# Optimization experiments

Hardware: AMD Instinct MI355X
Metric: run time of the kernel (lower is better)

## Reference

```python
import jax, jax.numpy as jnp
import numpy as np

B, T, F, D, H, L, DFF, G = 4, 2048, 512, 1024, 16, 2, 4096, 16
WSCALE = 0.03  # ~1/sqrt(D) so activations stay well-conditioned


def setup_inputs() -> dict:
    key = jax.random.key(0)
    ks = iter(jax.random.split(key, 24))

    def w(shape):
        return jax.random.normal(next(ks), shape, jnp.float32) * WSCALE

    return {
        "x": jax.random.normal(next(ks), (B, T, F), jnp.float32),
        "proj_w": w((D, F)), "proj_b": jnp.zeros((D,), jnp.float32),
        "wq": w((L, D, D)), "wk": w((L, D, D)), "wv": w((L, D, D)),
        "bq": jnp.zeros((L, D), jnp.float32), "bk": jnp.zeros((L, D), jnp.float32), "bv": jnp.zeros((L, D), jnp.float32),
        "wo": w((L, D, D)), "bo": jnp.zeros((L, D), jnp.float32),
        "ln1_g": jnp.ones((L, D), jnp.float32), "ln1_b": jnp.zeros((L, D), jnp.float32),
        "ln2_g": jnp.ones((L, D), jnp.float32), "ln2_b": jnp.zeros((L, D), jnp.float32),
        "w1": w((L, DFF, D)), "b1": jnp.zeros((L, DFF), jnp.float32),
        "w2": w((L, D, DFF)), "b2": jnp.zeros((L, D), jnp.float32),
        "hw1": w((G, D, D)), "hb1": jnp.zeros((G, D), jnp.float32),
        "hw2": w((G, 2, D)), "hb2": jnp.zeros((G, 2), jnp.float32),
        "nhead": H,
    }


def _ln(x, g, b, eps=1e-5):
    m = x.mean(-1, keepdims=True)
    v = ((x - m) ** 2).mean(-1, keepdims=True)
    return (x - m) * jax.lax.rsqrt(v + eps) * g + b


def _pe(t, d):
    # sinusoidal positional encoding, shape (t, d) (d even -> sin/cos interleave)
    pos = jnp.arange(t, dtype=jnp.float32)[:, None]
    div = jnp.exp(jnp.arange(0, d, 2, dtype=jnp.float32) * (-np.log(10000.0) / d))
    ph = pos * div
    return jnp.stack([jnp.sin(ph), jnp.cos(ph)], axis=-1).reshape(t, d)


def reference(x, proj_w, proj_b, wq, wk, wv, bq, bk, bv, wo, bo,
              ln1_g, ln1_b, ln2_g, ln2_b, w1, b1, w2, b2,
              hw1, hb1, hw2, hb2, nhead):
    Bx, Tx, _ = x.shape
    Dm = proj_w.shape[0]
    dh = Dm // nhead
    h = x @ proj_w.T + proj_b + _pe(Tx, Dm)  # (B,T,D)
    for l in range(wq.shape[0]):  # post-norm encoder layers
        q = (h @ wq[l].T + bq[l]).reshape(Bx, Tx, nhead, dh)
        k = (h @ wk[l].T + bk[l]).reshape(Bx, Tx, nhead, dh)
        v = (h @ wv[l].T + bv[l]).reshape(Bx, Tx, nhead, dh)
        # explicit (non-fused) attention path, as forced by need_weights=True
        scores = jnp.einsum('bthd,bshd->bhts', q, k) / jnp.sqrt(jnp.float32(dh))
        attn = jax.nn.softmax(scores, axis=-1)  # (B,H,T,T)
        ctx = jnp.einsum('bhts,bshd->bthd', attn, v).reshape(Bx, Tx, Dm)
        h = _ln(h + ctx @ wo[l].T + bo[l], ln1_g[l], ln1_b[l])
        ff = jax.nn.relu(h @ w1[l].T + b1[l]) @ w2[l].T + b2[l]
        h = _ln(h + ff, ln2_g[l], ln2_b[l])
    hl = h[:, -1, :]  # last-token pooling, (B,D)
    z = jax.nn.relu(jnp.einsum('bd,gkd->bgk', hl, hw1) + hb1)  # per-sector hidden
    logits = jnp.einsum('bgk,gok->bgo', z, hw2) + hb2           # (B,G,2)
    return jax.nn.softmax(logits, axis=-1)
```

## Files before the change

### kernel.cpp

```cpp
#include <hip/hip_runtime.h>
#include <hip/hip_bf16.h>
#include <cstdint>
#include <cstddef>


typedef __bf16 bf16_t;
typedef __attribute__((ext_vector_type(8))) __bf16 bf16x8;
typedef __attribute__((ext_vector_type(4))) __bf16 bf16x4;
typedef __attribute__((ext_vector_type(4))) float f32x4;
typedef __attribute__((ext_vector_type(16))) float f32x16;
typedef __attribute__((ext_vector_type(2))) unsigned u32x2;
typedef __attribute__((ext_vector_type(4))) unsigned u32x4;

#define DEV __device__ __forceinline__
#define AS1 __attribute__((address_space(1)))
#define AS3 __attribute__((address_space(3)))

DEV void gload_lds16(const void* g, void* l) {
  __builtin_amdgcn_global_load_lds((AS1 void*)(g), (AS3 void*)(l), 16, 0, 0);
}

DEV const char* swz_ptr(const void* base, int row, int colb) {
  return (const char*)base + row * 128 + ((((colb >> 4) ^ (row & 7))) << 4) +
         (colb & 15);
}

DEV unsigned cvtpk(float lo, float hi) {
  unsigned r;
  asm("v_cvt_pk_bf16_f32 %0, %1, %2" : "=v"(r) : "v"(lo), "v"(hi));
  return r;
}
DEV void swap32(unsigned& a, unsigned& b) {
  u32x2 r = __builtin_amdgcn_permlane32_swap(a, b, false, false);
  a = r[0];
  b = r[1];
}
DEV bf16x8 mkfrag(unsigned w0, unsigned w1, unsigned w2, unsigned w3) {
  u32x4 v = {w0, w1, w2, w3};
  return __builtin_bit_cast(bf16x8, v);
}

__global__ __launch_bounds__(256) void f2b_kernel(const float* __restrict__ s,
                                                  bf16_t* __restrict__ d, int n4) {
  const int i = blockIdx.x * 256 + threadIdx.x;
  if (i >= n4) return;
  const float4 v = *(const float4*)&s[(size_t)i * 4];
  bf16x4 o = {(bf16_t)v.x, (bf16_t)v.y, (bf16_t)v.z, (bf16_t)v.w};
  *(bf16x4*)&d[(size_t)i * 4] = o;
}

__global__ __launch_bounds__(256) void bcat_kernel(const float* __restrict__ bq,
                                                   const float* __restrict__ bk,
                                                   const float* __restrict__ bv,
                                                   float* __restrict__ out) {
  const int idx = blockIdx.x * 256 + threadIdx.x;
  const int l = idx / 3072, r = idx - l * 3072;
  const int p = r >> 10, i = r & 1023;
  const float* s = (p == 0) ? bq : ((p == 1) ? bk : bv);
  out[idx] = s[l * 1024 + i];
}

__global__ __launch_bounds__(256) void pe_kernel(float* __restrict__ pe) {
  const int idx = blockIdx.x * 256 + threadIdx.x;
  const int t = idx >> 9, i = idx & 511;
  const float dv = __expf((float)(2 * i) * -0.008994473019508785f);
  const float ph = (float)t * dv;
  pe[(size_t)t * 1024 + 2 * i] = sinf(ph);
  pe[(size_t)t * 1024 + 2 * i + 1] = cosf(ph);
}

template <int EPI, int BM, int BN>
__global__ __launch_bounds__(BM == 256 ? 512 : 256, 2) void gemm9(
    const bf16_t* __restrict__ A, const bf16_t* __restrict__ W,
    const float* __restrict__ bias, bf16_t* __restrict__ outb,
    float* __restrict__ outf, const float* __restrict__ res32,
    const float* __restrict__ pe, int M, int N, int K) {
  constexpr int T = (BM == 256) ? 512 : 256;
  constexpr int RPC = T / 8;
  constexpr int NA = (BM * 128) / (T * 16);
  constexpr int NB = (BN * 128) / (T * 16);
  constexpr int LPT = NA + NB;
  constexpr bool WIDE = (BM == 256 && BN == 256);
  constexpr int MF = WIDE ? 8 : 4;
  constexpr int ASZ = BM * 128;
  constexpr int BUFSZ = (BM + BN) * 128;
  __shared__ char smem[2][BUFSZ];
  const int tid = threadIdx.x, wv = tid >> 6, ln = tid & 63;
  const int nwg = gridDim.x * gridDim.y;
  int bid = blockIdx.y * gridDim.x + blockIdx.x;
  bid = (bid & 7) * (nwg >> 3) + (bid >> 3);
  const int m0 = (bid / gridDim.x) * BM, n0 = (bid % gridDim.x) * BN;
  const int wrow = WIDE ? (wv >> 2) * 128 : (wv >> 1) * 64;
  const int wcol = WIDE ? (wv & 3) * 64 : (wv & 1) * 64;
  f32x4 acc[MF][4] = {};

  const int tp = tid ^ ((tid >> 3) & 7);
  const int srow = tp >> 3, sc8 = (tp & 7) * 8;
  const bf16_t* pa[NA];
  const bf16_t* pb[NB];
#pragma unroll
  for (int u = 0; u < NA; ++u) pa[u] = A + (size_t)(m0 + u * RPC + srow) * K + sc8;
#pragma unroll
  for (int u = 0; u < NB; ++u) pb[u] = W + (size_t)(n0 + u * RPC + srow) * K + sc8;
  const int wvb = wv * 1024;

  auto stage = [&](int s) {
    char* bA = &smem[s][0] + wvb;
    char* bB = &smem[s][ASZ] + wvb;
#pragma unroll
    for (int u = 0; u < NA; ++u) {
      gload_lds16(pa[u], bA + u * (T * 16));
      pa[u] += 64;
    }
#pragma unroll
    for (int u = 0; u < NB; ++u) {
      gload_lds16(pb[u], bB + u * (T * 16));
      pb[u] += 64;
    }
  };

  auto wait_lpt = [&]() {
    if constexpr (LPT == 8)
      asm volatile("s_waitcnt vmcnt(8)" ::: "memory");
    else
      asm volatile("s_waitcnt vmcnt(6)" ::: "memory");
  };

  const int NK = K >> 6;
  stage(0);
  stage(1);
  wait_lpt();
  __builtin_amdgcn_s_barrier();

  for (int kt = 0; kt < NK; ++kt) {
    const char* bA = &smem[kt & 1][0];
    const char* bB = &smem[kt & 1][ASZ];
#pragma unroll
    for (int ks = 0; ks < 2; ++ks) {
      const int cb = ks * 64 + (ln >> 4) * 16;
      bf16x8 bF[4];
#pragma unroll
      for (int n = 0; n < 4; ++n) {
        const int lb = (wcol + n * 16 + (ln & 15)) * 128 + cb;
        bF[n] = *(const bf16x8*)(bB + (lb ^ (((lb >> 7) & 7) << 4)));
      }
#pragma unroll
      for (int mh = 0; mh < 2; ++mh) {
        bf16x8 aF[MF / 2];
#pragma unroll
        for (int m = 0; m < MF / 2; ++m) {
          const int lb = (wrow + (mh * (MF / 2) + m) * 16 + (ln & 15)) * 128 + cb;
          aF[m] = *(const bf16x8*)(bA + (lb ^ (((lb >> 7) & 7) << 4)));
        }
        __builtin_amdgcn_s_setprio(1);
#pragma unroll
        for (int m = 0; m < MF / 2; ++m)
#pragma unroll
          for (int n = 0; n < 4; ++n)
            acc[mh * (MF / 2) + m][n] = __builtin_amdgcn_mfma_f32_16x16x32_bf16(
                aF[m], bF[n], acc[mh * (MF / 2) + m][n], 0, 0, 0);
        __builtin_amdgcn_s_setprio(0);
      }
    }
    __builtin_amdgcn_s_barrier();
    if (kt + 2 < NK) {
      stage(kt & 1);
      wait_lpt();
    } else if (kt + 1 < NK) {
      asm volatile("s_waitcnt vmcnt(0)" ::: "memory");
    }
    __builtin_amdgcn_s_barrier();
    __builtin_amdgcn_sched_barrier(0);
  }

  const int rr = (ln >> 4) * 4, cc = ln & 15;
#pragma unroll
  for (int m = 0; m < MF; ++m) {
    const int rowb = m0 + wrow + m * 16 + rr;
#pragma unroll
    for (int n = 0; n < 4; ++n) {
      const int col = n0 + wcol + n * 16 + cc;
      const float bv = bias[col];
#pragma unroll
      for (int r = 0; r < 4; ++r) {
        const int row = rowb + r;
        float v = acc[m][n][r] + bv;
        const size_t o = (size_t)row * N + col;
        if constexpr (EPI == 1) {
          v = fmaxf(v, 0.f);
          outb[o] = (bf16_t)v;
        } else if constexpr (EPI == 2) {
          v += pe[(size_t)(row & 2047) * 1024 + col];
          outb[o] = (bf16_t)v;
          outf[o] = v;
        } else if constexpr (EPI == 3) {
          v += res32[o];
          outf[o] = v;
        } else {
          outb[o] = (bf16_t)v;
        }
      }
    }
  }
}

__global__ __launch_bounds__(256) void ln_kernel(const float* __restrict__ pre,
                                                 const float* __restrict__ g,
                                                 const float* __restrict__ b,
                                                 bf16_t* __restrict__ h16,
                                                 float* __restrict__ h32) {
  const int row = blockIdx.x, tid = threadIdx.x;
  const size_t base = (size_t)row * 1024 + tid * 4;
  const float4 v = *(const float4*)&pre[base];
  float s = v.x + v.y + v.z + v.w;
  float s2 = v.x * v.x + v.y * v.y + v.z * v.z + v.w * v.w;
#pragma unroll
  for (int m = 1; m < 64; m <<= 1) {
    s += __shfl_xor(s, m);
    s2 += __shfl_xor(s2, m);
  }
  __shared__ float ls[4], ls2[4];
  if ((tid & 63) == 0) {
    ls[tid >> 6] = s;
    ls2[tid >> 6] = s2;
  }
  __syncthreads();
  s = ls[0] + ls[1] + ls[2] + ls[3];
  s2 = ls2[0] + ls2[1] + ls2[2] + ls2[3];
  const float mean = s * (1.f / 1024.f);
  const float var = s2 * (1.f / 1024.f) - mean * mean;
  const float rs = rsqrtf(var + 1e-5f);
  const float4 gv = *(const float4*)&g[tid * 4];
  const float4 bv = *(const float4*)&b[tid * 4];
  const float o0 = (v.x - mean) * rs * gv.x + bv.x;
  const float o1 = (v.y - mean) * rs * gv.y + bv.y;
  const float o2 = (v.z - mean) * rs * gv.z + bv.z;
  const float o3 = (v.w - mean) * rs * gv.w + bv.w;
  bf16x4 ob = {(bf16_t)o0, (bf16_t)o1, (bf16_t)o2, (bf16_t)o3};
  *(bf16x4*)&h16[base] = ob;
  float4 of = {o0, o1, o2, o3};
  *(float4*)&h32[base] = of;
}

__global__ __launch_bounds__(256) void transpose_v(const bf16_t* __restrict__ v,
                                                   bf16_t* __restrict__ vt) {
  __shared__ bf16_t tile[64][80];
  const int bh = blockIdx.y, t0 = blockIdx.x * 64;
  const int tid = threadIdx.x;
  const int b = bh >> 4;
  const size_t vbase = ((size_t)(b * 2048 + t0)) * 3072 + (bh & 15) * 64;
#pragma unroll
  for (int p = 0; p < 2; ++p) {
    const int chunk = p * 256 + tid;
    const int tr = chunk >> 3, c8 = (chunk & 7) * 8;
    *(bf16x8*)&tile[tr][c8] = *(const bf16x8*)&v[vbase + (size_t)tr * 3072 + c8];
  }
  __syncthreads();
  const int d = tid >> 2, t8 = (tid & 3) * 16;
  bf16_t tmp[16];
#pragma unroll
  for (int j = 0; j < 16; ++j) tmp[j] = tile[t8 + j][d];
  const size_t obase = ((size_t)bh * 64 + d) * 2048 + t0 + t8;
  *(bf16x8*)&vt[obase] = *(bf16x8*)&tmp[0];
  *(bf16x8*)&vt[obase + 8] = *(bf16x8*)&tmp[8];
}

__global__ __launch_bounds__(256, 4) void attn_kernel(const bf16_t* __restrict__ qkv,
                                                      const bf16_t* __restrict__ vt,
                                                      bf16_t* __restrict__ ctx) {
  constexpr float SCL = 0.18033688011112042f;
  constexpr int QS = 3072;
  __shared__ bf16_t lK[2][64 * 64];
  __shared__ bf16_t lV[2][64 * 64];
  const int tid = threadIdx.x, wv = tid >> 6, ln = tid & 63;
  const int nwg = gridDim.x * gridDim.y;
  int bid = blockIdx.y * gridDim.x + blockIdx.x;
  bid = (bid & 7) * (nwg >> 3) + (bid >> 3);
  const int bh = bid / gridDim.x, b = bh >> 4, h = bh & 15;
  const int q0 = (bid % gridDim.x) * 128 + wv * 32;
  const int lq = ln & 31, hi = ln >> 5;
  const bf16_t* qp = qkv + (size_t)(b * 2048 + q0 + lq) * QS + h * 64 + hi * 8;
  bf16x8 qF[4];
#pragma unroll
  for (int kk = 0; kk < 4; ++kk) qF[kk] = *(const bf16x8*)(qp + kk * 16);
  f32x16 O0 = {}, O1 = {};
  float m_q = -1e30f, l_q = 0.f;
  const int sr = tid >> 3;
  const int scS = ((tid & 7) ^ ((tid >> 3) & 7)) * 8;
  const bf16_t* kp0 = qkv + 1024 + (size_t)(b * 2048 + sr) * QS + h * 64 + scS;
  const bf16_t* kp1 = kp0 + (size_t)32 * QS;
  const bf16_t* vp0 = vt + (size_t)bh * 64 * 2048 + (size_t)sr * 2048 + scS;
  const bf16_t* vp1 = vp0 + 32 * 2048;

  auto stage = [&](int bufi) {
    char* dk = (char*)&lK[bufi][0] + wv * 1024;
    char* dv = (char*)&lV[bufi][0] + wv * 1024;
    gload_lds16(kp0, dk);
    gload_lds16(kp1, dk + 4096);
    gload_lds16(vp0, dv);
    gload_lds16(vp1, dv + 4096);
    kp0 += (size_t)64 * QS;
    kp1 += (size_t)64 * QS;
    vp0 += 64;
    vp1 += 64;
  };

  stage(0);
  asm volatile("s_waitcnt vmcnt(0)" ::: "memory");
  __builtin_amdgcn_s_barrier();

  for (int st = 0; st < 32; ++st) {
    const int cur = st & 1;
    if (st + 1 < 32) stage(cur ^ 1);
#pragma unroll
    for (int sb = 0; sb < 2; ++sb) {
      f32x16 s = {};
      __builtin_amdgcn_s_setprio(1);
#pragma unroll
      for (int kk = 0; kk < 4; ++kk) {
        const bf16x8 kf =
            *(const bf16x8*)swz_ptr(&lK[cur][0], sb * 32 + lq, kk * 32 + hi * 16);
        s = __builtin_amdgcn_mfma_f32_32x32x16_bf16(kf, qF[kk], s, 0, 0, 0);
      }
      __builtin_amdgcn_s_setprio(0);
      float t0 = fmaxf(fmaxf(s[0], s[1]), fmaxf(s[2], s[3]));
      float t1 = fmaxf(fmaxf(s[4], s[5]), fmaxf(s[6], s[7]));
      float t2 = fmaxf(fmaxf(s[8], s[9]), fmaxf(s[10], s[11]));
      float t3 = fmaxf(fmaxf(s[12], s[13]), fmaxf(s[14], s[15]));
      float mx = fmaxf(fmaxf(t0, t1), fmaxf(t2, t3)) * SCL;
      mx = fmaxf(mx, __shfl_xor(mx, 32));
      if (__any(mx > m_q + 8.f)) {
        const float mnew = fmaxf(m_q, mx);
        const float alpha = exp2f(m_q - mnew);
        m_q = mnew;
        l_q *= alpha;
#pragma unroll
        for (int r = 0; r < 16; ++r) {
          const float ar = __shfl(alpha, (r & 3) + 8 * (r >> 2) + 4 * hi);
          O0[r] *= ar;
          O1[r] *= ar;
        }
      }
      float ra = 0.f, rb = 0.f;
#pragma unroll
      for (int i = 0; i < 8; ++i) {
        s[i] = exp2f(fmaf(s[i], SCL, -m_q));
        ra += s[i];
        s[i + 8] = exp2f(fmaf(s[i + 8], SCL, -m_q));
        rb += s[i + 8];
      }
      float rsum = ra + rb;
      rsum += __shfl_xor(rsum, 32);
      l_q += rsum;
      unsigned A = cvtpk(s[0], s[1]), Bq = cvtpk(s[2], s[3]);
      unsigned C = cvtpk(s[4], s[5]), Dq = cvtpk(s[6], s[7]);
      unsigned A2 = cvtpk(s[8], s[9]), B2 = cvtpk(s[10], s[11]);
      unsigned C2 = cvtpk(s[12], s[13]), D2 = cvtpk(s[14], s[15]);
      swap32(A, C);
      swap32(Bq, Dq);
      swap32(A2, C2);
      swap32(B2, D2);
      const bf16x8 f0 = mkfrag(A, Bq, C, Dq);
      const bf16x8 f1 = mkfrag(A2, B2, C2, D2);
      __builtin_amdgcn_s_setprio(1);
      const bf16x8 va = *(const bf16x8*)swz_ptr(&lV[cur][0], lq, sb * 64 + hi * 16);
      const bf16x8 vb =
          *(const bf16x8*)swz_ptr(&lV[cur][0], lq, sb * 64 + 32 + hi * 16);
      const bf16x8 vc =
          *(const bf16x8*)swz_ptr(&lV[cur][0], 32 + lq, sb * 64 + hi * 16);
      const bf16x8 vd =
          *(const bf16x8*)swz_ptr(&lV[cur][0], 32 + lq, sb * 64 + 32 + hi * 16);
      O0 = __builtin_amdgcn_mfma_f32_32x32x16_bf16(f0, va, O0, 0, 0, 0);
      O0 = __builtin_amdgcn_mfma_f32_32x32x16_bf16(f1, vb, O0, 0, 0, 0);
      O1 = __builtin_amdgcn_mfma_f32_32x32x16_bf16(f0, vc, O1, 0, 0, 0);
      O1 = __builtin_amdgcn_mfma_f32_32x32x16_bf16(f1, vd, O1, 0, 0, 0);
      __builtin_amdgcn_s_setprio(0);
    }
    asm volatile("s_waitcnt vmcnt(0)" ::: "memory");
    __builtin_amdgcn_s_barrier();
    __builtin_amdgcn_sched_barrier(0);
  }
  const float invl = 1.f / l_q;
  const size_t obase = ((size_t)(b * 2048 + q0)) * 1024 + h * 64 + lq;
#pragma unroll
  for (int r = 0; r < 16; ++r) {
    const int qr = (r & 3) + 8 * (r >> 2) + 4 * hi;
    const float iv = __shfl(invl, qr);
    ctx[obase + (size_t)qr * 1024] = (bf16_t)(O0[r] * iv);
    ctx[obase + (size_t)qr * 1024 + 32] = (bf16_t)(O1[r] * iv);
  }
}

__global__ __launch_bounds__(256) void head_z(const float* __restrict__ h32,
                                              const float* __restrict__ hw1,
                                              const float* __restrict__ hb1,
                                              float* __restrict__ z) {
  const int g = blockIdx.x, slab = blockIdx.y;
  const int wv = threadIdx.x >> 6, ln = threadIdx.x & 63;
  float4 hl[4][4];
#pragma unroll
  for (int b = 0; b < 4; ++b)
#pragma unroll
    for (int c = 0; c < 4; ++c)
      hl[b][c] = *(const float4*)&h32[((size_t)b * 2048 + 2047) * 1024 + c * 256 + ln * 4];
  const int k0 = slab * 64 + wv * 16;
  for (int kk = 0; kk < 16; ++kk) {
    const int kq = k0 + kk;
    const float* wrow = hw1 + ((size_t)g * 1024 + kq) * 1024;
    float p[4] = {0, 0, 0, 0};
#pragma unroll
    for (int c = 0; c < 4; ++c) {
      const float4 w4 = *(const float4*)&wrow[c * 256 + ln * 4];
#pragma unroll
      for (int b = 0; b < 4; ++b)
        p[b] += w4.x * hl[b][c].x + w4.y * hl[b][c].y + w4.z * hl[b][c].z +
                w4.w * hl[b][c].w;
    }
#pragma unroll
    for (int m = 1; m < 64; m <<= 1)
#pragma unroll
      for (int b = 0; b < 4; ++b) p[b] += __shfl_xor(p[b], m);
    if (ln == 0) {
#pragma unroll
      for (int b = 0; b < 4; ++b)
        z[((size_t)b * 16 + g) * 1024 + kq] = fmaxf(p[b] + hb1[g * 1024 + kq], 0.f);
    }
  }
}

__global__ __launch_bounds__(64) void head_logits(const float* __restrict__ z,
                                                  const float* __restrict__ hw2,
                                                  const float* __restrict__ hb2,
                                                  float* __restrict__ out) {
  const int b = blockIdx.x, g = blockIdx.y, ln = threadIdx.x;
  const float* zr = z + ((size_t)b * 16 + g) * 1024;
  const float* w0 = hw2 + (size_t)g * 2048;
  const float* w1 = w0 + 1024;
  float p0 = 0.f, p1 = 0.f;
#pragma unroll
  for (int c = 0; c < 4; ++c) {
    const float4 zv = *(const float4*)&zr[c * 256 + ln * 4];
    const float4 a0 = *(const float4*)&w0[c * 256 + ln * 4];
    const float4 a1 = *(const float4*)&w1[c * 256 + ln * 4];
    p0 += zv.x * a0.x + zv.y * a0.y + zv.z * a0.z + zv.w * a0.w;
    p1 += zv.x * a1.x + zv.y * a1.y + zv.z * a1.z + zv.w * a1.w;
  }
#pragma unroll
  for (int m = 1; m < 64; m <<= 1) {
    p0 += __shfl_xor(p0, m);
    p1 += __shfl_xor(p1, m);
  }
  if (ln == 0) {
    const float l0 = p0 + hb2[g * 2], l1 = p1 + hb2[g * 2 + 1];
    const float mx = fmaxf(l0, l1);
    const float e0 = expf(l0 - mx), e1 = expf(l1 - mx);
    const float inv = 1.f / (e0 + e1);
    out[(size_t)b * 32 + g * 2] = e0 * inv;
    out[(size_t)b * 32 + g * 2 + 1] = e1 * inv;
  }
}

extern "C" void kernel_launch(void* const* d_in, const int* in_sizes, int n_in,
                              void* d_out, int out_size, void* d_ws, size_t ws_size,
                              hipStream_t stream) {
  const float* x = (const float*)d_in[0];
  const float* proj_w = (const float*)d_in[1];
  const float* proj_b = (const float*)d_in[2];
  const float* wq = (const float*)d_in[3];
  const float* wk = (const float*)d_in[4];
  const float* wvv = (const float*)d_in[5];
  const float* bq = (const float*)d_in[6];
  const float* bk = (const float*)d_in[7];
  const float* bv = (const float*)d_in[8];
  const float* wo = (const float*)d_in[9];
  const float* bo = (const float*)d_in[10];
  const float* ln1_g = (const float*)d_in[11];
  const float* ln1_b = (const float*)d_in[12];
  const float* ln2_g = (const float*)d_in[13];
  const float* ln2_b = (const float*)d_in[14];
  const float* w1 = (const float*)d_in[15];
  const float* b1 = (const float*)d_in[16];
  const float* w2 = (const float*)d_in[17];
  const float* b2 = (const float*)d_in[18];
  const float* hw1 = (const float*)d_in[19];
  const float* hb1 = (const float*)d_in[20];
  const float* hw2 = (const float*)d_in[21];
  const float* hb2 = (const float*)d_in[22];
  float* out = (float*)d_out;
  char* ws = (char*)d_ws;

  size_t o = 0;
  auto take = [&](size_t bytes) { size_t r = o; o += bytes; return r; };
  const size_t o_wqkv = take(12582912);
  const size_t o_wo = take(4194304);
  const size_t o_w1 = take(16777216);
  const size_t o_w2 = take(16777216);
  const size_t o_pw = take(1048576);
  const size_t o_h16 = take(16777216);
  const size_t o_h32 = take(33554432);
  const size_t o_pre = take(33554432);
  const size_t o_r4 = take(67108864);
  const size_t o_r5 = take(16777216);
  const size_t o_z = take(262144);
  const size_t o_bqkv = take(24576);

  bf16_t* wqkv16 = (bf16_t*)(ws + o_wqkv);
  bf16_t* wo16 = (bf16_t*)(ws + o_wo);
  bf16_t* w1_16 = (bf16_t*)(ws + o_w1);
  bf16_t* w2_16 = (bf16_t*)(ws + o_w2);
  bf16_t* pw16 = (bf16_t*)(ws + o_pw);
  bf16_t* h16 = (bf16_t*)(ws + o_h16);
  float* h32 = (float*)(ws + o_h32);
  float* pre32 = (float*)(ws + o_pre);
  bf16_t* qkv16 = (bf16_t*)(ws + o_r4);
  bf16_t* vT16 = (bf16_t*)(ws + o_r4 + 50331648);
  bf16_t* ff1 = (bf16_t*)(ws + o_r4);
  bf16_t* x16 = (bf16_t*)(ws + o_r5);
  float* pe32 = (float*)(ws + o_r5 + 8388608);
  bf16_t* ctx16 = (bf16_t*)(ws + o_r5);
  float* zbuf = (float*)(ws + o_z);
  float* bqkv = (float*)(ws + o_bqkv);

  f2b_kernel<<<4096, 256, 0, stream>>>(x, x16, 1048576);
  f2b_kernel<<<512, 256, 0, stream>>>(proj_w, pw16, 131072);
  for (int l = 0; l < 2; ++l) {
    f2b_kernel<<<1024, 256, 0, stream>>>(wq + (size_t)l * 1048576,
                                         wqkv16 + (size_t)(l * 3 + 0) * 1048576, 262144);
    f2b_kernel<<<1024, 256, 0, stream>>>(wk + (size_t)l * 1048576,
                                         wqkv16 + (size_t)(l * 3 + 1) * 1048576, 262144);
    f2b_kernel<<<1024, 256, 0, stream>>>(wvv + (size_t)l * 1048576,
                                         wqkv16 + (size_t)(l * 3 + 2) * 1048576, 262144);
  }
  f2b_kernel<<<2048, 256, 0, stream>>>(wo, wo16, 524288);
  f2b_kernel<<<8192, 256, 0, stream>>>(w1, w1_16, 2097152);
  f2b_kernel<<<8192, 256, 0, stream>>>(w2, w2_16, 2097152);
  bcat_kernel<<<24, 256, 0, stream>>>(bq, bk, bv, bqkv);
  pe_kernel<<<4096, 256, 0, stream>>>(pe32);

  gemm9<2, 128, 128><<<dim3(8, 64), 256, 0, stream>>>(x16, pw16, proj_b, h16, h32,
                                                      nullptr, pe32, 8192, 1024, 512);

  for (int l = 0; l < 2; ++l) {
    const bf16_t* wqkv_l = wqkv16 + (size_t)l * 3145728;
    const bf16_t* wo_l = wo16 + (size_t)l * 1048576;
    const bf16_t* w1_l = w1_16 + (size_t)l * 4194304;
    const bf16_t* w2_l = w2_16 + (size_t)l * 4194304;

    gemm9<0, 256, 128><<<dim3(24, 32), 512, 0, stream>>>(h16, wqkv_l, bqkv + l * 3072,
                                                         qkv16, nullptr, nullptr,
                                                         nullptr, 8192, 3072, 1024);
    transpose_v<<<dim3(32, 64), 256, 0, stream>>>(qkv16 + 2048, vT16);
    attn_kernel<<<dim3(16, 64), 256, 0, stream>>>(qkv16, vT16, ctx16);
    gemm9<3, 128, 128><<<dim3(8, 64), 256, 0, stream>>>(ctx16, wo_l, bo + l * 1024,
                                                        nullptr, pre32, h32, nullptr,
                                                        8192, 1024, 1024);
    ln_kernel<<<8192, 256, 0, stream>>>(pre32, ln1_g + l * 1024, ln1_b + l * 1024, h16,
                                        h32);
    gemm9<1, 256, 256><<<dim3(16, 32), 512, 0, stream>>>(h16, w1_l, b1 + l * 4096, ff1,
                                                         nullptr, nullptr, nullptr,
                                                         8192, 4096, 1024);
    gemm9<3, 128, 128><<<dim3(8, 64), 256, 0, stream>>>(ff1, w2_l, b2 + l * 1024,
                                                        nullptr, pre32, h32, nullptr,
                                                        8192, 1024, 4096);
    ln_kernel<<<8192, 256, 0, stream>>>(pre32, ln2_g + l * 1024, ln2_b + l * 1024, h16,
                                        h32);
  }

  head_z<<<dim3(16, 16), 256, 0, stream>>>(h32, hw1, hb1, zbuf);
  head_logits<<<dim3(4, 16), 64, 0, stream>>>(zbuf, hw2, hb2, out);
}
```

Before: 884.3 us.

## Load all LDS fragments before barrier and overlap next-stage prefetch with MFMAs

The GEMM kernel now reads all A/B fragments for both k-substeps from LDS into registers, waits on lgkmcnt, barriers, then issues the next global->LDS stage before running the MFMA block. The goal is to overlap global loads with compute instead of serializing them after the MFMAs. The wide 256x256 tile variant is removed and the FFN1 GEMM now uses 256x128 tiles with twice the grid. Holding all fragments at once raises register pressure, and the smaller FFN1 tile costs more operand traffic per output.

```diff
diff --git a/kernel.cpp b/kernel.cpp
--- a/kernel.cpp
+++ b/kernel.cpp
@@ -70,7 +70,7 @@
 }
 
 template <int EPI, int BM, int BN>
-__global__ __launch_bounds__(BM == 256 ? 512 : 256, 2) void gemm9(
+__global__ __launch_bounds__(BM == 256 ? 512 : 256, 2) void gemm10(
     const bf16_t* __restrict__ A, const bf16_t* __restrict__ W,
     const float* __restrict__ bias, bf16_t* __restrict__ outb,
     float* __restrict__ outf, const float* __restrict__ res32,
@@ -80,8 +80,6 @@
   constexpr int NA = (BM * 128) / (T * 16);
   constexpr int NB = (BN * 128) / (T * 16);
   constexpr int LPT = NA + NB;
-  constexpr bool WIDE = (BM == 256 && BN == 256);
-  constexpr int MF = WIDE ? 8 : 4;
   constexpr int ASZ = BM * 128;
   constexpr int BUFSZ = (BM + BN) * 128;
   __shared__ char smem[2][BUFSZ];
@@ -90,9 +88,9 @@
   int bid = blockIdx.y * gridDim.x + blockIdx.x;
   bid = (bid & 7) * (nwg >> 3) + (bid >> 3);
   const int m0 = (bid / gridDim.x) * BM, n0 = (bid % gridDim.x) * BN;
-  const int wrow = WIDE ? (wv >> 2) * 128 : (wv >> 1) * 64;
-  const int wcol = WIDE ? (wv & 3) * 64 : (wv & 1) * 64;
-  f32x4 acc[MF][4] = {};
+  const int wrow = (wv >> 1) * 64;
+  const int wcol = (wv & 1) * 64;
+  f32x4 acc[4][4] = {};
 
   const int tp = tid ^ ((tid >> 3) & 7);
   const int srow = tp >> 3, sc8 = (tp & 7) * 8;
@@ -135,36 +133,37 @@
   for (int kt = 0; kt < NK; ++kt) {
     const char* bA = &smem[kt & 1][0];
     const char* bB = &smem[kt & 1][ASZ];
+    bf16x8 aF[2][4], bF[2][4];
 #pragma unroll
     for (int ks = 0; ks < 2; ++ks) {
       const int cb = ks * 64 + (ln >> 4) * 16;
-      bf16x8 bF[4];
+#pragma unroll
+      for (int m = 0; m < 4; ++m) {
+        const int lb = (wrow + m * 16 + (ln & 15)) * 128 + cb;
+        aF[ks][m] = *(const bf16x8*)(bA + (lb ^ (((lb >> 7) & 7) << 4)));
+      }
 #pragma unroll
       for (int n = 0; n < 4; ++n) {
         const int lb = (wcol + n * 16 + (ln & 15)) * 128 + cb;
-        bF[n] = *(const bf16x8*)(bB + (lb ^ (((lb >> 7) & 7) << 4)));
+        bF[ks][n] = *(const bf16x8*)(bB + (lb ^ (((lb >> 7) & 7) << 4)));
       }
-#pragma unroll
-      for (int mh = 0; mh < 2; ++mh) {
-        bf16x8 aF[MF / 2];
-#pragma unroll
-        for (int m = 0; m < MF / 2; ++m) {
-          const int lb = (wrow + (mh * (MF / 2) + m) * 16 + (ln & 15)) * 128 + cb;
-          aF[m] = *(const bf16x8*)(bA + (lb ^ (((lb >> 7) & 7) << 4)));
-        }
-        __builtin_amdgcn_s_setprio(1);
-#pragma unroll
-        for (int m = 0; m < MF / 2; ++m)
-#pragma unroll
-          for (int n = 0; n < 4; ++n)
-            acc[mh * (MF / 2) + m][n] = __builtin_amdgcn_mfma_f32_16x16x32_bf16(
-                aF[m], bF[n], acc[mh * (MF / 2) + m][n], 0, 0, 0);
-        __builtin_amdgcn_s_setprio(0);
-      }
-    }
+    }
+    asm volatile("s_waitcnt lgkmcnt(0)" ::: "memory");
+    __builtin_amdgcn_sched_barrier(0);
     __builtin_amdgcn_s_barrier();
+    __builtin_amdgcn_sched_barrier(0);
+    if (kt + 2 < NK) stage(kt & 1);
+    __builtin_amdgcn_s_setprio(1);
+#pragma unroll
+    for (int ks = 0; ks < 2; ++ks)
+#pragma unroll
+      for (int m = 0; m < 4; ++m)
+#pragma unroll
+        for (int n = 0; n < 4; ++n)
+          acc[m][n] = __builtin_amdgcn_mfma_f32_16x16x32_bf16(aF[ks][m], bF[ks][n],
+                                                              acc[m][n], 0, 0, 0);
+    __builtin_amdgcn_s_setprio(0);
     if (kt + 2 < NK) {
-      stage(kt & 1);
       wait_lpt();
     } else if (kt + 1 < NK) {
       asm volatile("s_waitcnt vmcnt(0)" ::: "memory");
@@ -175,7 +174,7 @@
 
   const int rr = (ln >> 4) * 4, cc = ln & 15;
 #pragma unroll
-  for (int m = 0; m < MF; ++m) {
+  for (int m = 0; m < 4; ++m) {
     const int rowb = m0 + wrow + m * 16 + rr;
 #pragma unroll
     for (int n = 0; n < 4; ++n) {
@@ -537,8 +536,8 @@
   bcat_kernel<<<24, 256, 0, stream>>>(bq, bk, bv, bqkv);
   pe_kernel<<<4096, 256, 0, stream>>>(pe32);
 
-  gemm9<2, 128, 128><<<dim3(8, 64), 256, 0, stream>>>(x16, pw16, proj_b, h16, h32,
-                                                      nullptr, pe32, 8192, 1024, 512);
+  gemm10<2, 128, 128><<<dim3(8, 64), 256, 0, stream>>>(x16, pw16, proj_b, h16, h32,
+                                                       nullptr, pe32, 8192, 1024, 512);
 
   for (int l = 0; l < 2; ++l) {
     const bf16_t* wqkv_l = wqkv16 + (size_t)l * 3145728;
@@ -546,22 +545,22 @@
     const bf16_t* w1_l = w1_16 + (size_t)l * 4194304;
     const bf16_t* w2_l = w2_16 + (size_t)l * 4194304;
 
-    gemm9<0, 256, 128><<<dim3(24, 32), 512, 0, stream>>>(h16, wqkv_l, bqkv + l * 3072,
-                                                         qkv16, nullptr, nullptr,
-                                                         nullptr, 8192, 3072, 1024);
+    gemm10<0, 256, 128><<<dim3(24, 32), 512, 0, stream>>>(h16, wqkv_l, bqkv + l * 3072,
+                                                          qkv16, nullptr, nullptr,
+                                                          nullptr, 8192, 3072, 1024);
     transpose_v<<<dim3(32, 64), 256, 0, stream>>>(qkv16 + 2048, vT16);
     attn_kernel<<<dim3(16, 64), 256, 0, stream>>>(qkv16, vT16, ctx16);
-    gemm9<3, 128, 128><<<dim3(8, 64), 256, 0, stream>>>(ctx16, wo_l, bo + l * 1024,
-                                                        nullptr, pre32, h32, nullptr,
-                                                        8192, 1024, 1024);
+    gemm10<3, 128, 128><<<dim3(8, 64), 256, 0, stream>>>(ctx16, wo_l, bo + l * 1024,
+                                                         nullptr, pre32, h32, nullptr,
+                                                         8192, 1024, 1024);
     ln_kernel<<<8192, 256, 0, stream>>>(pre32, ln1_g + l * 1024, ln1_b + l * 1024, h16,
                                         h32);
-    gemm9<1, 256, 256><<<dim3(16, 32), 512, 0, stream>>>(h16, w1_l, b1 + l * 4096, ff1,
-                                                         nullptr, nullptr, nullptr,
-                                                         8192, 4096, 1024);
-    gemm9<3, 128, 128><<<dim3(8, 64), 256, 0, stream>>>(ff1, w2_l, b2 + l * 1024,
-                                                        nullptr, pre32, h32, nullptr,
-                                                        8192, 1024, 4096);
+    gemm10<1, 256, 128><<<dim3(32, 32), 512, 0, stream>>>(h16, w1_l, b1 + l * 4096, ff1,
+                                                          nullptr, nullptr, nullptr,
+                                                          8192, 4096, 1024);
+    gemm10<3, 128, 128><<<dim3(8, 64), 256, 0, stream>>>(ff1, w2_l, b2 + l * 1024,
+                                                         nullptr, pre32, h32, nullptr,
+                                                         8192, 1024, 4096);
     ln_kernel<<<8192, 256, 0, stream>>>(pre32, ln2_g + l * 1024, ln2_b + l * 1024, h16,
                                         h32);
   }
```

Result: no change. 891.5 us (+0.8%).
